# Kernel tuning notes

Hardware: AMD Instinct MI355X
Metric: run time of the kernel (lower is better)

The kernel has to match this reference:

```python
import jax, jax.numpy as jnp
import numpy as np

B, S, I, H, E, V = 32, 128, 1024, 1024, 1024, 32000


def setup_inputs() -> dict:
    key = jax.random.key(0)
    ks = jax.random.split(key, 16)
    s = 0.02
    return {
        "x": jax.random.normal(ks[0], (1, B, I), jnp.float32),
        "encoder_outputs": jax.random.normal(ks[1], (S, B, E), jnp.float32),
        "hidden": jax.random.normal(ks[2], (1, B, H), jnp.float32),
        # GRU params (torch layout: gates r, z, n stacked)
        "W_ih": jax.random.normal(ks[3], (3 * H, I), jnp.float32) * s,
        "W_hh": jax.random.normal(ks[4], (3 * H, H), jnp.float32) * s,
        "b_ih": jnp.zeros((3 * H,), jnp.float32),
        "b_hh": jnp.zeros((3 * H,), jnp.float32),
        # attn: Linear(hidden + enc_hidden -> hidden)
        "W_attn": jax.random.normal(ks[5], (H, H + E), jnp.float32) * s,
        "b_attn": jnp.zeros((H,), jnp.float32),
        # attn_combine: Linear(input + enc_hidden -> input)
        "W_comb": jax.random.normal(ks[6], (I, I + E), jnp.float32) * s,
        "b_comb": jnp.zeros((I,), jnp.float32),
        # out: Linear(hidden -> vocab)
        "W_out": jax.random.normal(ks[7], (V, H), jnp.float32) * s,
        "b_out": jnp.zeros((V,), jnp.float32),
    }


def reference(x, encoder_outputs, hidden,
              W_ih, W_hh, b_ih, b_hh,
              W_attn, b_attn, W_comb, b_comb, W_out, b_out):
    Hd = hidden.shape[-1]
    x0, h0 = x[0], hidden[0]                     # [B,I], [B,H]
    # --- single GRU step (torch gate order r, z, n) ---
    xg = x0 @ W_ih.T + b_ih                      # [B,3H]
    hg = h0 @ W_hh.T + b_hh                      # [B,3H]
    r = jax.nn.sigmoid(xg[:, :Hd] + hg[:, :Hd])
    z = jax.nn.sigmoid(xg[:, Hd:2 * Hd] + hg[:, Hd:2 * Hd])
    n = jnp.tanh(xg[:, 2 * Hd:] + r * hg[:, 2 * Hd:])
    dec = (1.0 - z) * n + z * h0                 # [B,H] decoder_output
    # --- batched Bahdanau-style score: dec_b . attn([dec_b; enc_sb]) ---
    Sn = encoder_outputs.shape[0]
    dec_rep = jnp.broadcast_to(dec[None], (Sn,) + dec.shape)      # [S,B,H]
    cat = jnp.concatenate([dec_rep, encoder_outputs], axis=-1)    # [S,B,H+E]
    proj = jnp.einsum('sbc,hc->sbh', cat, W_attn) + b_attn        # [S,B,H]
    scores = jnp.einsum('bh,sbh->bs', dec, proj)                  # [B,S]
    attn_weights = jax.nn.softmax(scores, axis=-1)                # [B,S]
    context = jnp.einsum('bs,sbe->be', attn_weights, encoder_outputs)  # [B,E]
    # --- combine input + context, project to vocab, log-softmax ---
    comb = jnp.concatenate([x0, context], axis=-1) @ W_comb.T + b_comb  # [B,I]
    output = jax.nn.log_softmax(comb @ W_out.T + b_out, axis=-1)        # [B,V]
    return output, attn_weights
```

## Files before the change

kernel.cpp:

```cpp
#include <hip/hip_runtime.h>
#include <hip/hip_bf16.h>
#include <math.h>

#define BDIM 32
#define HD   1024
#define SD   128
#define VD   32000

typedef __attribute__((ext_vector_type(8))) short short8;
typedef __attribute__((ext_vector_type(4))) float floatx4;

__device__ __forceinline__ short f2bf(float f) {
    unsigned u = __builtin_bit_cast(unsigned, f);
    u += 0x7FFFu + ((u >> 16) & 1u);
    return (short)(u >> 16);
}
__device__ __forceinline__ float bf2f(short h) {
    unsigned u = ((unsigned)(unsigned short)h) << 16;
    return __builtin_bit_cast(float, u);
}
__device__ __forceinline__ unsigned pack2(float a, float b) {
    unsigned ua = __builtin_bit_cast(unsigned, a) + 0x8000u;
    unsigned ub = __builtin_bit_cast(unsigned, b) + 0x8000u;
    return (ub & 0xffff0000u) | (ua >> 16);
}

__device__ __forceinline__ size_t swz_idx(int b, int k) {
    int t = k >> 5, q = (k & 31) >> 3, j = k & 7;
    int mt = b >> 4, i = b & 15;
    return ((size_t)(((t * 2 + mt) * 64) + q * 16 + i) << 3) + j;
}

#define MFMA(a, b, c) __builtin_amdgcn_mfma_f32_16x16x32_bf16(a, b, c, 0, 0, 0)

__global__ __launch_bounds__(256) void prep0(
    const float* __restrict__ x0, const float* __restrict__ h0,
    const float* __restrict__ b_ih, const float* __restrict__ b_hh,
    const float* __restrict__ b_comb,
    float* __restrict__ xg, float* __restrict__ hg,
    float* __restrict__ v, float* __restrict__ sexp,
    float* __restrict__ comb,
    short* __restrict__ x0h, short* __restrict__ x0l,
    short* __restrict__ h0h, short* __restrict__ h0l,
    short* __restrict__ cath)
{
    int idx = blockIdx.x * 256 + threadIdx.x;
    if (idx < 98304) { xg[idx] = b_ih[idx % 3072]; return; }
    idx -= 98304;
    if (idx < 98304) { hg[idx] = b_hh[idx % 3072]; return; }
    idx -= 98304;
    if (idx < 32768) { v[idx] = 0.f; return; }
    idx -= 32768;
    if (idx < 32) { sexp[idx] = 0.f; return; }
    idx -= 32;
    if (idx < 32768) { comb[idx] = b_comb[idx & 1023]; return; }
    idx -= 32768;
    if (idx < 32768) {
        int b = idx >> 10, k = idx & 1023;
        float xv = x0[idx]; short hh = f2bf(xv);
        size_t d = swz_idx(b, k);
        x0h[d] = hh; x0l[d] = f2bf(xv - bf2f(hh)); cath[d] = hh;
        return;
    }
    idx -= 32768;
    if (idx < 32768) {
        int b = idx >> 10, k = idx & 1023;
        float xv = h0[idx]; short hh = f2bf(xv);
        size_t d = swz_idx(b, k);
        h0h[d] = hh; h0l[d] = f2bf(xv - bf2f(hh));
    }
}

template<int ATOMIC, int SPLIT, int KCHUNK>
__device__ __forceinline__ void gemm_bt_body(
    const short* __restrict__ bhi, const short* __restrict__ blo,
    const float* __restrict__ W, const float* __restrict__ bias,
    float* __restrict__ out, int N, int K, int k0)
{
    int tid = threadIdx.x;
    int w = tid >> 6, l = tid & 63;
    int i = l & 15, q = l >> 4;
    int n0 = blockIdx.x * 64 + w * 16;
    const float* wrow = W + (size_t)(n0 + i) * K + q * 8;
    const short8* bph = (const short8*)bhi + l;
    const short8* bpl = (const short8*)blo + l;

    floatx4 acc0 = {0.f, 0.f, 0.f, 0.f};
    floatx4 acc1 = {0.f, 0.f, 0.f, 0.f};

#pragma unroll 2
    for (int kk = k0; kk < k0 + KCHUNK; kk += 32) {
        float4 w0 = *(const float4*)(wrow + kk);
        float4 w1 = *(const float4*)(wrow + kk + 4);
        float wf[8] = {w0.x, w0.y, w0.z, w0.w, w1.x, w1.y, w1.z, w1.w};
        short8 ahi, alo;
#pragma unroll
        for (int j = 0; j < 8; ++j) {
            short hh = f2bf(wf[j]);
            ahi[j] = hh;
            if (SPLIT) alo[j] = f2bf(wf[j] - bf2f(hh));
        }
        int t2 = (kk >> 5) * 2;
        short8 b0 = bph[(size_t)t2 * 64];
        short8 b1 = bph[(size_t)(t2 + 1) * 64];
        acc0 = MFMA(ahi, b0, acc0);
        acc1 = MFMA(ahi, b1, acc1);
        if (SPLIT) {
            short8 l0 = bpl[(size_t)t2 * 64];
            short8 l1 = bpl[(size_t)(t2 + 1) * 64];
            acc0 = MFMA(ahi, l0, acc0);
            acc1 = MFMA(ahi, l1, acc1);
            acc0 = MFMA(alo, b0, acc0);
            acc1 = MFMA(alo, b1, acc1);
        }
    }

    __shared__ float lds[4][32][17];
#pragma unroll
    for (int r = 0; r < 4; ++r) {
        lds[w][i][q * 4 + r]      = acc0[r];
        lds[w][i + 16][q * 4 + r] = acc1[r];
    }
    __syncthreads();
    int b = l >> 1, hf = l & 1;
    float vo[8];
#pragma unroll
    for (int t = 0; t < 8; ++t) vo[t] = lds[w][b][hf * 8 + t];
    size_t obase = (size_t)b * N + n0 + hf * 8;
    if (ATOMIC) {
#pragma unroll
        for (int t = 0; t < 8; ++t) atomicAdd(out + obase + t, vo[t]);
    } else {
        const float4* bp4 = (const float4*)(bias + n0 + hf * 8);
        float4 bb0 = bp4[0], bb1 = bp4[1];
        float4 o0 = {vo[0] + bb0.x, vo[1] + bb0.y, vo[2] + bb0.z, vo[3] + bb0.w};
        float4 o1 = {vo[4] + bb1.x, vo[5] + bb1.y, vo[6] + bb1.z, vo[7] + bb1.w};
        float4* op = (float4*)(out + obase);
        op[0] = o0; op[1] = o1;
    }
}

__global__ __launch_bounds__(256) void gemm_gates(
    const short* __restrict__ x0h, const short* __restrict__ x0l,
    const short* __restrict__ h0h, const short* __restrict__ h0l,
    const float* __restrict__ W_ih, const float* __restrict__ W_hh,
    float* __restrict__ xg, float* __restrict__ hg)
{
    if (blockIdx.z == 0)
        gemm_bt_body<1, 1, 512>(x0h, x0l, W_ih, nullptr, xg, 3072, 1024,
                                blockIdx.y * 512);
    else
        gemm_bt_body<1, 1, 512>(h0h, h0l, W_hh, nullptr, hg, 3072, 1024,
                                blockIdx.y * 512);
}

__global__ __launch_bounds__(256) void gemm_comb_k(
    const short* __restrict__ cath, const float* __restrict__ W_comb,
    float* __restrict__ comb)
{
    gemm_bt_body<1, 0, 256>(cath, nullptr, W_comb, nullptr, comb, 1024, 2048,
                            blockIdx.y * 256);
}

__global__ __launch_bounds__(256) void gru_gate(
    const float* __restrict__ xg, const float* __restrict__ hg,
    const float* __restrict__ h0, short* __restrict__ dh, short* __restrict__ dl)
{
    int idx = blockIdx.x * 256 + threadIdx.x;
    int b = idx >> 10, h = idx & 1023;
    const float* xp = xg + (size_t)b * 3072 + h;
    const float* hp = hg + (size_t)b * 3072 + h;
    float r = 1.f / (1.f + expf(-(xp[0] + hp[0])));
    float z = 1.f / (1.f + expf(-(xp[1024] + hp[1024])));
    float n = tanhf(xp[2048] + r * hp[2048]);
    float dec = (1.f - z) * n + z * h0[idx];
    short hh = f2bf(dec);
    size_t d = swz_idx(b, h);
    dh[d] = hh; dl[d] = f2bf(dec - bf2f(hh));
}

__global__ __launch_bounds__(256) void gemm_attn2(
    const short* __restrict__ dhi, const short* __restrict__ dlo,
    const float* __restrict__ Wa, float* __restrict__ v)
{
    int tid = threadIdx.x, w = tid >> 6, l = tid & 63;
    int i = l & 15, q = l >> 4;
    int e0 = blockIdx.x * 64;
    int k0 = blockIdx.y * 128;
    __shared__ float lds[32][65];

    const short8* ah = (const short8*)dhi;
    const short8* al = (const short8*)dlo;
    short8 Ah[4][2], Al[4][2];
#pragma unroll
    for (int t = 0; t < 4; ++t)
#pragma unroll
        for (int mt = 0; mt < 2; ++mt) {
            size_t idx = (size_t)((((k0 >> 5) + t) * 2 + mt) * 64) + l;
            Ah[t][mt] = ah[idx]; Al[t][mt] = al[idx];
        }

    floatx4 acc[2] = {{0.f,0.f,0.f,0.f},{0.f,0.f,0.f,0.f}};
    int sr = tid >> 3;
    int sc_ = (tid & 7) * 8;
#pragma unroll
    for (int t = 0; t < 4; ++t) {
        const float* src = Wa + (size_t)(k0 + t * 32 + sr) * 2048 + 1024 + e0 + sc_;
        float4 s0 = *(const float4*)src;
        float4 s1 = *(const float4*)(src + 4);
        __syncthreads();
        *(float4*)&lds[sr][sc_]     = s0;
        *(float4*)&lds[sr][sc_ + 4] = s1;
        __syncthreads();
        short8 Bh, Bl;
#pragma unroll
        for (int j = 0; j < 8; ++j) {
            float f = lds[q * 8 + j][w * 16 + i];
            unsigned u = __builtin_bit_cast(unsigned, f);
            float hif = __builtin_bit_cast(float, u & 0xffff0000u);
            Bh[j] = (short)(u >> 16);
            float lo = f - hif;
            Bl[j] = (short)(__builtin_bit_cast(unsigned, lo) >> 16);
        }
        acc[0] = MFMA(Ah[t][0], Bh, acc[0]);
        acc[1] = MFMA(Ah[t][1], Bh, acc[1]);
        acc[0] = MFMA(Ah[t][0], Bl, acc[0]);
        acc[1] = MFMA(Ah[t][1], Bl, acc[1]);
        acc[0] = MFMA(Al[t][0], Bh, acc[0]);
        acc[1] = MFMA(Al[t][1], Bh, acc[1]);
    }
#pragma unroll
    for (int mt = 0; mt < 2; ++mt)
#pragma unroll
        for (int r = 0; r < 4; ++r)
            atomicAdd(v + (size_t)(mt * 16 + q * 4 + r) * 1024 + e0 + w * 16 + i,
                      acc[mt][r]);
}

__global__ __launch_bounds__(256) void scores_k(
    const float* __restrict__ v, const float* __restrict__ enc,
    float* __restrict__ sc)
{
    int w = threadIdx.x >> 6, l = threadIdx.x & 63;
    int id = blockIdx.x * 4 + w;
    int s = id >> 5, b = id & 31;
    const float4* ep = (const float4*)(enc + ((size_t)s * BDIM + b) * 1024);
    const float4* vp = (const float4*)(v + (size_t)b * 1024);
    float acc = 0.f;
#pragma unroll
    for (int c = 0; c < 4; ++c) {
        float4 e4 = ep[l + 64 * c];
        float4 v4 = vp[l + 64 * c];
        acc += e4.x * v4.x + e4.y * v4.y + e4.z * v4.z + e4.w * v4.w;
    }
    for (int o = 32; o; o >>= 1) acc += __shfl_down(acc, o);
    if (l == 0) sc[b * SD + s] = acc;
}

__global__ __launch_bounds__(256) void ctx_softmax(
    const float* __restrict__ sc, const float* __restrict__ enc,
    short* __restrict__ cath, float* __restrict__ aw_out)
{
    int b = blockIdx.y, tid = threadIdx.x;
    int w = tid >> 6, l = tid & 63;
    __shared__ float a[SD];
    __shared__ float red[8];
    float x = (tid < SD) ? sc[b * SD + tid] : -3.4e38f;
    float m = x;
    for (int o = 32; o; o >>= 1) m = fmaxf(m, __shfl_down(m, o));
    if (l == 0) red[w] = m;
    __syncthreads();
    float M = fmaxf(fmaxf(red[0], red[1]), fmaxf(red[2], red[3]));
    float e = (tid < SD) ? __expf(x - M) : 0.f;
    float su = e;
    for (int o = 32; o; o >>= 1) su += __shfl_down(su, o);
    if (l == 0) red[4 + w] = su;
    __syncthreads();
    float S = red[4] + red[5] + red[6] + red[7];
    if (tid < SD) {
        float aw = e / S;
        a[tid] = aw;
        if (blockIdx.x == 0) aw_out[b * SD + tid] = aw;
    }
    __syncthreads();
    int ecol = blockIdx.x * 256 + tid;
    const float* p = enc + (size_t)b * 1024 + ecol;
    float acc = 0.f;
#pragma unroll 4
    for (int s = 0; s < SD; ++s) acc += a[s] * p[(size_t)s * (BDIM * 1024)];
    unsigned u = __builtin_bit_cast(unsigned, acc) + 0x8000u;
    cath[swz_idx(b, 1024 + ecol)] = (short)(u >> 16);
}

__global__ __launch_bounds__(256) void comb_prep(
    const float* __restrict__ comb, short* __restrict__ ch)
{
    int idx = blockIdx.x * 256 + threadIdx.x;
    int b = idx >> 10, k = idx & 1023;
    ch[swz_idx(b, k)] = f2bf(comb[idx]);
}

__global__ __launch_bounds__(256) void gemm_out_k(
    const short* __restrict__ combh, const float* __restrict__ W,
    const float* __restrict__ bias, float* __restrict__ out,
    float* __restrict__ sexp)
{
    int tid = threadIdx.x, w = tid >> 6, l = tid & 63;
    int i = l & 15, q = l >> 4;
    int n0 = blockIdx.x * 64 + w * 16;
    const float* wrow = W + (size_t)(n0 + i) * 1024 + q * 8;
    const short8* bp = (const short8*)combh + l;
    floatx4 acc0 = {0.f, 0.f, 0.f, 0.f};
    floatx4 acc1 = {0.f, 0.f, 0.f, 0.f};
#pragma unroll 4
    for (int kk = 0; kk < 1024; kk += 32) {
        float4 w0 = *(const float4*)(wrow + kk);
        float4 w1 = *(const float4*)(wrow + kk + 4);
        union { unsigned u[4]; short8 s; } pk;
        pk.u[0] = pack2(w0.x, w0.y);
        pk.u[1] = pack2(w0.z, w0.w);
        pk.u[2] = pack2(w1.x, w1.y);
        pk.u[3] = pack2(w1.z, w1.w);
        int t2 = (kk >> 5) * 2;
        short8 b0 = bp[(size_t)t2 * 64];
        short8 b1 = bp[(size_t)(t2 + 1) * 64];
        acc0 = MFMA(pk.s, b0, acc0);
        acc1 = MFMA(pk.s, b1, acc1);
    }
    __shared__ float lds[4][32][17];
    __shared__ float bsum[32];
    if (tid < 32) bsum[tid] = 0.f;
#pragma unroll
    for (int r = 0; r < 4; ++r) {
        lds[w][i][q * 4 + r]      = acc0[r];
        lds[w][i + 16][q * 4 + r] = acc1[r];
    }
    __syncthreads();
    int b = l >> 1, hf = l & 1;
    float vo[8];
#pragma unroll
    for (int t = 0; t < 8; ++t) vo[t] = lds[w][b][hf * 8 + t];
    const float4* bp4 = (const float4*)(bias + n0 + hf * 8);
    float4 bb0 = bp4[0], bb1 = bp4[1];
    vo[0] += bb0.x; vo[1] += bb0.y; vo[2] += bb0.z; vo[3] += bb0.w;
    vo[4] += bb1.x; vo[5] += bb1.y; vo[6] += bb1.z; vo[7] += bb1.w;
    float es = 0.f;
#pragma unroll
    for (int t = 0; t < 8; ++t) es += __expf(vo[t]);
    atomicAdd(&bsum[b], es);
    float4 o0 = {vo[0], vo[1], vo[2], vo[3]};
    float4 o1 = {vo[4], vo[5], vo[6], vo[7]};
    float4* op = (float4*)(out + (size_t)b * VD + n0 + hf * 8);
    op[0] = o0; op[1] = o1;
    __syncthreads();
    if (tid < 32) atomicAdd(sexp + tid, bsum[tid]);
}

__global__ __launch_bounds__(256) void final_k(
    float* __restrict__ out, const float* __restrict__ sexp)
{
    int b = blockIdx.y;
    int vv = blockIdx.x * 256 + threadIdx.x;
    size_t o = (size_t)b * VD + vv;
    out[o] -= logf(sexp[b]);
}

extern "C" void kernel_launch(void* const* d_in, const int* in_sizes, int n_in,
                              void* d_out, int out_size, void* d_ws, size_t ws_size,
                              hipStream_t stream) {
    const float* x      = (const float*)d_in[0];
    const float* enc    = (const float*)d_in[1];
    const float* hid    = (const float*)d_in[2];
    const float* W_ih   = (const float*)d_in[3];
    const float* W_hh   = (const float*)d_in[4];
    const float* b_ih   = (const float*)d_in[5];
    const float* b_hh   = (const float*)d_in[6];
    const float* W_attn = (const float*)d_in[7];
    const float* W_comb = (const float*)d_in[9];
    const float* b_comb = (const float*)d_in[10];
    const float* W_out  = (const float*)d_in[11];
    const float* b_out  = (const float*)d_in[12];
    float* out = (float*)d_out;

    float* wsf   = (float*)d_ws;
    float* xg    = wsf;
    float* hg    = xg + 98304;
    float* v     = hg + 98304;
    float* sexp  = v + 32768;
    float* comb  = sexp + 32;
    float* sc    = comb + 32768;
    short* x0h   = (short*)(sc + 4096);
    short* x0l   = x0h + 32768;
    short* h0h   = x0l + 32768;
    short* h0l   = h0h + 32768;
    short* dh    = h0l + 32768;
    short* dl    = dh + 32768;
    short* cath  = dl + 32768;
    short* combh = cath + 65536;

    prep0<<<1281, 256, 0, stream>>>(x, hid, b_ih, b_hh, b_comb,
                                    xg, hg, v, sexp, comb,
                                    x0h, x0l, h0h, h0l, cath);
    gemm_gates<<<dim3(48, 2, 2), 256, 0, stream>>>(
        x0h, x0l, h0h, h0l, W_ih, W_hh, xg, hg);
    gru_gate<<<128, 256, 0, stream>>>(xg, hg, hid, dh, dl);
    gemm_attn2<<<dim3(16, 8), 256, 0, stream>>>(dh, dl, W_attn, v);
    scores_k<<<1024, 256, 0, stream>>>(v, enc, sc);
    ctx_softmax<<<dim3(4, 32), 256, 0, stream>>>(sc, enc, cath, out + 1024000);
    gemm_comb_k<<<dim3(16, 8), 256, 0, stream>>>(cath, W_comb, comb);
    comb_prep<<<128, 256, 0, stream>>>(comb, combh);
    gemm_out_k<<<500, 256, 0, stream>>>(combh, W_out, b_out, out, sexp);
    final_k<<<dim3(125, 32), 256, 0, stream>>>(out, sexp);
}
```

Baseline: 316.7 us.

## Fuse attention scores, softmax and context; fold prep kernels into GEMMs

Merges the score and context kernels into one pass. It takes exp of the raw scores with no max subtraction and accumulates both the numerator and the denominator with atomics. Attention normalization and the concat bf16 conversion move into the comb GEMM, and conversion of comb plus its bias moves into every block of the vocab GEMM's LDS. Zero-init moves to hipMemsetAsync and GRU biases are added inside gru_gate, removing the large prep kernel and comb_prep. In exchange, every one of the 500 output blocks redundantly converts the full comb matrix into 64KB of LDS, which can limit occupancy. Dropping the max subtraction also risks overflow for large scores.

```diff
diff --git a/kernel.cpp b/kernel.cpp
--- a/kernel.cpp
+++ b/kernel.cpp
@@ -25,57 +25,38 @@
     return (ub & 0xffff0000u) | (ua >> 16);
 }
 
-__device__ __forceinline__ size_t swz_idx(int b, int k) {
+__device__ __forceinline__ int swz_idx(int b, int k) {
     int t = k >> 5, q = (k & 31) >> 3, j = k & 7;
     int mt = b >> 4, i = b & 15;
-    return ((size_t)(((t * 2 + mt) * 64) + q * 16 + i) << 3) + j;
+    return ((((t * 2 + mt) * 64) + q * 16 + i) << 3) + j;
 }
 
 #define MFMA(a, b, c) __builtin_amdgcn_mfma_f32_16x16x32_bf16(a, b, c, 0, 0, 0)
 
-__global__ __launch_bounds__(256) void prep0(
+__global__ __launch_bounds__(256) void prep_swz(
     const float* __restrict__ x0, const float* __restrict__ h0,
-    const float* __restrict__ b_ih, const float* __restrict__ b_hh,
-    const float* __restrict__ b_comb,
-    float* __restrict__ xg, float* __restrict__ hg,
-    float* __restrict__ v, float* __restrict__ sexp,
-    float* __restrict__ comb,
     short* __restrict__ x0h, short* __restrict__ x0l,
-    short* __restrict__ h0h, short* __restrict__ h0l,
-    short* __restrict__ cath)
+    short* __restrict__ h0h, short* __restrict__ h0l)
 {
     int idx = blockIdx.x * 256 + threadIdx.x;
-    if (idx < 98304) { xg[idx] = b_ih[idx % 3072]; return; }
-    idx -= 98304;
-    if (idx < 98304) { hg[idx] = b_hh[idx % 3072]; return; }
-    idx -= 98304;
-    if (idx < 32768) { v[idx] = 0.f; return; }
-    idx -= 32768;
-    if (idx < 32) { sexp[idx] = 0.f; return; }
-    idx -= 32;
-    if (idx < 32768) { comb[idx] = b_comb[idx & 1023]; return; }
-    idx -= 32768;
     if (idx < 32768) {
         int b = idx >> 10, k = idx & 1023;
         float xv = x0[idx]; short hh = f2bf(xv);
-        size_t d = swz_idx(b, k);
-        x0h[d] = hh; x0l[d] = f2bf(xv - bf2f(hh)); cath[d] = hh;
-        return;
-    }
-    idx -= 32768;
-    if (idx < 32768) {
+        int d = swz_idx(b, k);
+        x0h[d] = hh; x0l[d] = f2bf(xv - bf2f(hh));
+    } else {
+        idx -= 32768;
         int b = idx >> 10, k = idx & 1023;
         float xv = h0[idx]; short hh = f2bf(xv);
-        size_t d = swz_idx(b, k);
+        int d = swz_idx(b, k);
         h0h[d] = hh; h0l[d] = f2bf(xv - bf2f(hh));
     }
 }
 
-template<int ATOMIC, int SPLIT, int KCHUNK>
-__device__ __forceinline__ void gemm_bt_body(
+template<int KCHUNK>
+__device__ __forceinline__ void gemm_gates_body(
     const short* __restrict__ bhi, const short* __restrict__ blo,
-    const float* __restrict__ W, const float* __restrict__ bias,
-    float* __restrict__ out, int N, int K, int k0)
+    const float* __restrict__ W, float* __restrict__ out, int N, int K, int k0)
 {
     int tid = threadIdx.x;
     int w = tid >> 6, l = tid & 63;
@@ -98,21 +79,19 @@
         for (int j = 0; j < 8; ++j) {
             short hh = f2bf(wf[j]);
             ahi[j] = hh;
-            if (SPLIT) alo[j] = f2bf(wf[j] - bf2f(hh));
+            alo[j] = f2bf(wf[j] - bf2f(hh));
         }
         int t2 = (kk >> 5) * 2;
         short8 b0 = bph[(size_t)t2 * 64];
         short8 b1 = bph[(size_t)(t2 + 1) * 64];
+        short8 l0 = bpl[(size_t)t2 * 64];
+        short8 l1 = bpl[(size_t)(t2 + 1) * 64];
         acc0 = MFMA(ahi, b0, acc0);
         acc1 = MFMA(ahi, b1, acc1);
-        if (SPLIT) {
-            short8 l0 = bpl[(size_t)t2 * 64];
-            short8 l1 = bpl[(size_t)(t2 + 1) * 64];
-            acc0 = MFMA(ahi, l0, acc0);
-            acc1 = MFMA(ahi, l1, acc1);
-            acc0 = MFMA(alo, b0, acc0);
-            acc1 = MFMA(alo, b1, acc1);
-        }
+        acc0 = MFMA(ahi, l0, acc0);
+        acc1 = MFMA(ahi, l1, acc1);
+        acc0 = MFMA(alo, b0, acc0);
+        acc1 = MFMA(alo, b1, acc1);
     }
 
     __shared__ float lds[4][32][17];
@@ -123,21 +102,9 @@
     }
     __syncthreads();
     int b = l >> 1, hf = l & 1;
-    float vo[8];
-#pragma unroll
-    for (int t = 0; t < 8; ++t) vo[t] = lds[w][b][hf * 8 + t];
     size_t obase = (size_t)b * N + n0 + hf * 8;
-    if (ATOMIC) {
-#pragma unroll
-        for (int t = 0; t < 8; ++t) atomicAdd(out + obase + t, vo[t]);
-    } else {
-        const float4* bp4 = (const float4*)(bias + n0 + hf * 8);
-        float4 bb0 = bp4[0], bb1 = bp4[1];
-        float4 o0 = {vo[0] + bb0.x, vo[1] + bb0.y, vo[2] + bb0.z, vo[3] + bb0.w};
-        float4 o1 = {vo[4] + bb1.x, vo[5] + bb1.y, vo[6] + bb1.z, vo[7] + bb1.w};
-        float4* op = (float4*)(out + obase);
-        op[0] = o0; op[1] = o1;
-    }
+#pragma unroll
+    for (int t = 0; t < 8; ++t) atomicAdd(out + obase + t, lds[w][b][hf * 8 + t]);
 }
 
 __global__ __launch_bounds__(256) void gemm_gates(
@@ -147,35 +114,28 @@
     float* __restrict__ xg, float* __restrict__ hg)
 {
     if (blockIdx.z == 0)
-        gemm_bt_body<1, 1, 512>(x0h, x0l, W_ih, nullptr, xg, 3072, 1024,
-                                blockIdx.y * 512);
+        gemm_gates_body<512>(x0h, x0l, W_ih, xg, 3072, 1024, blockIdx.y * 512);
     else
-        gemm_bt_body<1, 1, 512>(h0h, h0l, W_hh, nullptr, hg, 3072, 1024,
-                                blockIdx.y * 512);
-}
-
-__global__ __launch_bounds__(256) void gemm_comb_k(
-    const short* __restrict__ cath, const float* __restrict__ W_comb,
-    float* __restrict__ comb)
-{
-    gemm_bt_body<1, 0, 256>(cath, nullptr, W_comb, nullptr, comb, 1024, 2048,
-                            blockIdx.y * 256);
+        gemm_gates_body<512>(h0h, h0l, W_hh, hg, 3072, 1024, blockIdx.y * 512);
 }
 
 __global__ __launch_bounds__(256) void gru_gate(
     const float* __restrict__ xg, const float* __restrict__ hg,
-    const float* __restrict__ h0, short* __restrict__ dh, short* __restrict__ dl)
+    const float* __restrict__ h0,
+    const float* __restrict__ b_ih, const float* __restrict__ b_hh,
+    short* __restrict__ dh, short* __restrict__ dl)
 {
     int idx = blockIdx.x * 256 + threadIdx.x;
     int b = idx >> 10, h = idx & 1023;
     const float* xp = xg + (size_t)b * 3072 + h;
     const float* hp = hg + (size_t)b * 3072 + h;
-    float r = 1.f / (1.f + expf(-(xp[0] + hp[0])));
-    float z = 1.f / (1.f + expf(-(xp[1024] + hp[1024])));
-    float n = tanhf(xp[2048] + r * hp[2048]);
+    float r = 1.f / (1.f + __expf(-(xp[0] + b_ih[h] + hp[0] + b_hh[h])));
+    float z = 1.f / (1.f + __expf(-(xp[1024] + b_ih[1024 + h] +
+                                    hp[1024] + b_hh[1024 + h])));
+    float n = tanhf(xp[2048] + b_ih[2048 + h] + r * (hp[2048] + b_hh[2048 + h]));
     float dec = (1.f - z) * n + z * h0[idx];
     short hh = f2bf(dec);
-    size_t d = swz_idx(b, h);
+    int d = swz_idx(b, h);
     dh[d] = hh; dl[d] = f2bf(dec - bf2f(hh));
 }
 
@@ -237,79 +197,138 @@
                       acc[mt][r]);
 }
 
-__global__ __launch_bounds__(256) void scores_k(
+__global__ __launch_bounds__(256) void scores_ctx(
     const float* __restrict__ v, const float* __restrict__ enc,
-    float* __restrict__ sc)
-{
-    int w = threadIdx.x >> 6, l = threadIdx.x & 63;
-    int id = blockIdx.x * 4 + w;
-    int s = id >> 5, b = id & 31;
-    const float4* ep = (const float4*)(enc + ((size_t)s * BDIM + b) * 1024);
-    const float4* vp = (const float4*)(v + (size_t)b * 1024);
-    float acc = 0.f;
-#pragma unroll
-    for (int c = 0; c < 4; ++c) {
-        float4 e4 = ep[l + 64 * c];
-        float4 v4 = vp[l + 64 * c];
-        acc += e4.x * v4.x + e4.y * v4.y + e4.z * v4.z + e4.w * v4.w;
-    }
-    for (int o = 32; o; o >>= 1) acc += __shfl_down(acc, o);
-    if (l == 0) sc[b * SD + s] = acc;
-}
-
-__global__ __launch_bounds__(256) void ctx_softmax(
-    const float* __restrict__ sc, const float* __restrict__ enc,
-    short* __restrict__ cath, float* __restrict__ aw_out)
+    float* __restrict__ num, float* __restrict__ den, float* __restrict__ es)
 {
     int b = blockIdx.y, tid = threadIdx.x;
+    int s0 = blockIdx.x * 8;
     int w = tid >> 6, l = tid & 63;
-    __shared__ float a[SD];
-    __shared__ float red[8];
-    float x = (tid < SD) ? sc[b * SD + tid] : -3.4e38f;
-    float m = x;
-    for (int o = 32; o; o >>= 1) m = fmaxf(m, __shfl_down(m, o));
-    if (l == 0) red[w] = m;
-    __syncthreads();
-    float M = fmaxf(fmaxf(red[0], red[1]), fmaxf(red[2], red[3]));
-    float e = (tid < SD) ? __expf(x - M) : 0.f;
-    float su = e;
-    for (int o = 32; o; o >>= 1) su += __shfl_down(su, o);
-    if (l == 0) red[4 + w] = su;
-    __syncthreads();
-    float S = red[4] + red[5] + red[6] + red[7];
-    if (tid < SD) {
-        float aw = e / S;
-        a[tid] = aw;
-        if (blockIdx.x == 0) aw_out[b * SD + tid] = aw;
-    }
-    __syncthreads();
-    int ecol = blockIdx.x * 256 + tid;
-    const float* p = enc + (size_t)b * 1024 + ecol;
-    float acc = 0.f;
-#pragma unroll 4
-    for (int s = 0; s < SD; ++s) acc += a[s] * p[(size_t)s * (BDIM * 1024)];
-    unsigned u = __builtin_bit_cast(unsigned, acc) + 0x8000u;
-    cath[swz_idx(b, 1024 + ecol)] = (short)(u >> 16);
-}
-
-__global__ __launch_bounds__(256) void comb_prep(
-    const float* __restrict__ comb, short* __restrict__ ch)
-{
-    int idx = blockIdx.x * 256 + threadIdx.x;
-    int b = idx >> 10, k = idx & 1023;
-    ch[swz_idx(b, k)] = f2bf(comb[idx]);
-}
-
-__global__ __launch_bounds__(256) void gemm_out_k(
-    const short* __restrict__ combh, const float* __restrict__ W,
-    const float* __restrict__ bias, float* __restrict__ out,
-    float* __restrict__ sexp)
+    float4 vv = *((const float4*)(v + (size_t)b * 1024) + tid);
+    float4 e8[8];
+    float part[8];
+#pragma unroll
+    for (int s = 0; s < 8; ++s) {
+        float4 e4 = *((const float4*)(enc + ((size_t)(s0 + s) * BDIM + b) * 1024) + tid);
+        e8[s] = e4;
+        part[s] = e4.x * vv.x + e4.y * vv.y + e4.z * vv.z + e4.w * vv.w;
+    }
+    __shared__ float red[4][8];
+    __shared__ float esl[8];
+#pragma unroll
+    for (int s = 0; s < 8; ++s) {
+        float p = part[s];
+        for (int o = 32; o; o >>= 1) p += __shfl_down(p, o);
+        if (l == 0) red[w][s] = p;
+    }
+    __syncthreads();
+    if (tid < 8) {
+        float sc = red[0][tid] + red[1][tid] + red[2][tid] + red[3][tid];
+        float e = __expf(sc);
+        esl[tid] = e;
+        es[b * SD + s0 + tid] = e;
+    }
+    __syncthreads();
+    if (tid == 0) {
+        float ds = 0.f;
+#pragma unroll
+        for (int s = 0; s < 8; ++s) ds += esl[s];
+        atomicAdd(den + b, ds);
+    }
+    float n0 = 0.f, n1 = 0.f, n2 = 0.f, n3 = 0.f;
+#pragma unroll
+    for (int s = 0; s < 8; ++s) {
+        float e = esl[s];
+        n0 += e * e8[s].x; n1 += e * e8[s].y;
+        n2 += e * e8[s].z; n3 += e * e8[s].w;
+    }
+    float* np = num + (size_t)b * 1024 + tid * 4;
+    atomicAdd(np, n0); atomicAdd(np + 1, n1);
+    atomicAdd(np + 2, n2); atomicAdd(np + 3, n3);
+}
+
+__global__ __launch_bounds__(256) void gemm_comb2(
+    const float* __restrict__ x0, const float* __restrict__ num,
+    const float* __restrict__ den, const float* __restrict__ es,
+    const float* __restrict__ W_comb, float* __restrict__ comb,
+    float* __restrict__ aw_out)
+{
+    int tid = threadIdx.x;
+    int w = tid >> 6, l = tid & 63;
+    int i = l & 15, q = l >> 4;
+    int n0 = blockIdx.x * 64 + w * 16;
+    int k0 = blockIdx.y * 256;
+    __shared__ short cfrag[8192];
+
+    if (blockIdx.x == 0) {
+        int base = blockIdx.y * 512 + tid * 2;
+#pragma unroll
+        for (int j = 0; j < 2; ++j) {
+            int idx = base + j;
+            aw_out[idx] = es[idx] / den[idx >> 7];
+        }
+    }
+    for (int ii = tid; ii < 8192; ii += 256) {
+        int b = ii >> 8, kl = ii & 255;
+        int k = k0 + kl;
+        float xv = (k < 1024) ? x0[(b << 10) + k]
+                              : num[(b << 10) + (k & 1023)] / den[b];
+        cfrag[swz_idx(b, kl)] = f2bf(xv);
+    }
+    __syncthreads();
+
+    const float* wrow = W_comb + (size_t)(n0 + i) * 2048 + k0 + q * 8;
+    const short8* bp = (const short8*)cfrag + l;
+    floatx4 acc0 = {0.f, 0.f, 0.f, 0.f};
+    floatx4 acc1 = {0.f, 0.f, 0.f, 0.f};
+#pragma unroll 2
+    for (int kl = 0; kl < 256; kl += 32) {
+        float4 w0 = *(const float4*)(wrow + kl);
+        float4 w1 = *(const float4*)(wrow + kl + 4);
+        union { unsigned u[4]; short8 s; } pk;
+        pk.u[0] = pack2(w0.x, w0.y);
+        pk.u[1] = pack2(w0.z, w0.w);
+        pk.u[2] = pack2(w1.x, w1.y);
+        pk.u[3] = pack2(w1.z, w1.w);
+        int t2 = (kl >> 5) * 2;
+        short8 b0 = bp[t2 * 64];
+        short8 b1 = bp[(t2 + 1) * 64];
+        acc0 = MFMA(pk.s, b0, acc0);
+        acc1 = MFMA(pk.s, b1, acc1);
+    }
+    __shared__ float lds[4][32][17];
+#pragma unroll
+    for (int r = 0; r < 4; ++r) {
+        lds[w][i][q * 4 + r]      = acc0[r];
+        lds[w][i + 16][q * 4 + r] = acc1[r];
+    }
+    __syncthreads();
+    int b = l >> 1, hf = l & 1;
+    size_t obase = (size_t)b * 1024 + n0 + hf * 8;
+#pragma unroll
+    for (int t = 0; t < 8; ++t) atomicAdd(comb + obase + t, lds[w][b][hf * 8 + t]);
+}
+
+__global__ __launch_bounds__(256) void gemm_out2(
+    const float* __restrict__ comb, const float* __restrict__ b_comb,
+    const float* __restrict__ W, const float* __restrict__ bias,
+    float* __restrict__ out, float* __restrict__ sexp)
 {
     int tid = threadIdx.x, w = tid >> 6, l = tid & 63;
     int i = l & 15, q = l >> 4;
     int n0 = blockIdx.x * 64 + w * 16;
+    __shared__ short cfrag[32768];
+    __shared__ float lds[4][32][17];
+    __shared__ float bsum[32];
+    if (tid < 32) bsum[tid] = 0.f;
+    for (int ii = tid; ii < 32768; ii += 256) {
+        int b = ii >> 10, k = ii & 1023;
+        cfrag[swz_idx(b, k)] = f2bf(comb[ii] + b_comb[k]);
+    }
+    __syncthreads();
+
     const float* wrow = W + (size_t)(n0 + i) * 1024 + q * 8;
-    const short8* bp = (const short8*)combh + l;
+    const short8* bp = (const short8*)cfrag + l;
     floatx4 acc0 = {0.f, 0.f, 0.f, 0.f};
     floatx4 acc1 = {0.f, 0.f, 0.f, 0.f};
 #pragma unroll 4
@@ -322,14 +341,11 @@
         pk.u[2] = pack2(w1.x, w1.y);
         pk.u[3] = pack2(w1.z, w1.w);
         int t2 = (kk >> 5) * 2;
-        short8 b0 = bp[(size_t)t2 * 64];
-        short8 b1 = bp[(size_t)(t2 + 1) * 64];
+        short8 b0 = bp[t2 * 64];
+        short8 b1 = bp[(t2 + 1) * 64];
         acc0 = MFMA(pk.s, b0, acc0);
         acc1 = MFMA(pk.s, b1, acc1);
     }
-    __shared__ float lds[4][32][17];
-    __shared__ float bsum[32];
-    if (tid < 32) bsum[tid] = 0.f;
 #pragma unroll
     for (int r = 0; r < 4; ++r) {
         lds[w][i][q * 4 + r]      = acc0[r];
@@ -344,10 +360,10 @@
     float4 bb0 = bp4[0], bb1 = bp4[1];
     vo[0] += bb0.x; vo[1] += bb0.y; vo[2] += bb0.z; vo[3] += bb0.w;
     vo[4] += bb1.x; vo[5] += bb1.y; vo[6] += bb1.z; vo[7] += bb1.w;
-    float es = 0.f;
-#pragma unroll
-    for (int t = 0; t < 8; ++t) es += __expf(vo[t]);
-    atomicAdd(&bsum[b], es);
+    float esum = 0.f;
+#pragma unroll
+    for (int t = 0; t < 8; ++t) esum += __expf(vo[t]);
+    atomicAdd(&bsum[b], esum);
     float4 o0 = {vo[0], vo[1], vo[2], vo[3]};
     float4 o1 = {vo[4], vo[5], vo[6], vo[7]};
     float4* op = (float4*)(out + (size_t)b * VD + n0 + hf * 8);
@@ -382,33 +398,32 @@
     const float* b_out  = (const float*)d_in[12];
     float* out = (float*)d_out;
 
-    float* wsf   = (float*)d_ws;
-    float* xg    = wsf;
-    float* hg    = xg + 98304;
-    float* v     = hg + 98304;
-    float* sexp  = v + 32768;
-    float* comb  = sexp + 32;
-    float* sc    = comb + 32768;
-    short* x0h   = (short*)(sc + 4096);
-    short* x0l   = x0h + 32768;
-    short* h0h   = x0l + 32768;
-    short* h0l   = h0h + 32768;
-    short* dh    = h0l + 32768;
-    short* dl    = dh + 32768;
-    short* cath  = dl + 32768;
-    short* combh = cath + 65536;
-
-    prep0<<<1281, 256, 0, stream>>>(x, hid, b_ih, b_hh, b_comb,
-                                    xg, hg, v, sexp, comb,
-                                    x0h, x0l, h0h, h0l, cath);
+    float* wsf  = (float*)d_ws;
+    float* xg   = wsf;
+    float* hg   = xg + 98304;
+    float* v    = hg + 98304;
+    float* num  = v + 32768;
+    float* den  = num + 32768;
+    float* sexp = den + 32;
+    float* comb = sexp + 32;
+    size_t zcount = 98304u * 2 + 32768u * 3 + 64;
+    float* es   = comb + 32768;
+    short* x0h  = (short*)(es + 4096);
+    short* x0l  = x0h + 32768;
+    short* h0h  = x0l + 32768;
+    short* h0l  = h0h + 32768;
+    short* dh   = h0l + 32768;
+    short* dl   = dh + 32768;
+
+    hipMemsetAsync(wsf, 0, zcount * sizeof(float), stream);
+    prep_swz<<<256, 256, 0, stream>>>(x, hid, x0h, x0l, h0h, h0l);
     gemm_gates<<<dim3(48, 2, 2), 256, 0, stream>>>(
         x0h, x0l, h0h, h0l, W_ih, W_hh, xg, hg);
-    gru_gate<<<128, 256, 0, stream>>>(xg, hg, hid, dh, dl);
+    gru_gate<<<128, 256, 0, stream>>>(xg, hg, hid, b_ih, b_hh, dh, dl);
     gemm_attn2<<<dim3(16, 8), 256, 0, stream>>>(dh, dl, W_attn, v);
-    scores_k<<<1024, 256, 0, stream>>>(v, enc, sc);
-    ctx_softmax<<<dim3(4, 32), 256, 0, stream>>>(sc, enc, cath, out + 1024000);
-    gemm_comb_k<<<dim3(16, 8), 256, 0, stream>>>(cath, W_comb, comb);
-    comb_prep<<<128, 256, 0, stream>>>(comb, combh);
-    gemm_out_k<<<500, 256, 0, stream>>>(combh, W_out, b_out, out, sexp);
+    scores_ctx<<<dim3(16, 32), 256, 0, stream>>>(v, enc, num, den, es);
+    gemm_comb2<<<dim3(16, 8), 256, 0, stream>>>(
+        x, num, den, es, W_comb, comb, out + 1024000);
+    gemm_out2<<<500, 256, 0, stream>>>(comb, b_comb, W_out, b_out, out, sexp);
     final_k<<<dim3(125, 32), 256, 0, stream>>>(out, sexp);
 }
```

After: 347.7 us. 1.1x slower.
